# Kernel tuning notes

Hardware: AMD Instinct MI355X
Metric: run time of the kernel (lower is better)

## Reference

```python
import jax, jax.numpy as jnp
import numpy as np

B, W, D, R = 8, 1024, 1024, 64
GAMMA_MIN, GAMMA_MAX, ALPHA_CAP, EPS = 0.15, 1.0, 1.0, 1e-8


def _linear_init(key, fan_in, shape):
    bound = 1.0 / np.sqrt(fan_in)
    return jax.random.uniform(key, shape, jnp.float32, -bound, bound)


def setup_inputs() -> dict:
    key = jax.random.key(0)
    ks = jax.random.split(key, 12)
    h = jax.random.normal(ks[0], (B, W, D), jnp.float32)
    # k_base init as in __init__: exp(-0.15*max(j-i,0)) * tril, row-normalized
    pos = jnp.arange(W, dtype=jnp.float32)
    dist_ji = jnp.clip(pos[None, :] - pos[:, None], 0.0)
    causal = jnp.tril(jnp.ones((W, W), jnp.float32))
    k_init = jnp.exp(-0.15 * dist_ji) * causal
    k_base = k_init / jnp.clip(k_init.sum(axis=1, keepdims=True), 1e-8)
    # decay_logit init: gammas in [0.95, 0.995] -> inverse sigmoid of normalized gamma
    gammas = jnp.linspace(0.95, 0.995, R)
    graw = jnp.clip((gammas - GAMMA_MIN) / (GAMMA_MAX - GAMMA_MIN), 1e-6, 1 - 1e-6)
    decay_logit = jnp.log(graw / (1.0 - graw))
    return {
        "h": h,
        "k_base": k_base,
        "decay_logit": decay_logit,
        "gate_logit": jnp.asarray(8.0, jnp.float32),
        "alpha_logit": jnp.asarray(0.0, jnp.float32),
        "u": 0.05 * jax.random.normal(ks[1], (D, R), jnp.float32),
        "v": 0.05 * jax.random.normal(ks[2], (D, R), jnp.float32),
        "proj_w": _linear_init(ks[3], D, (D, D)),
        "proj_b": _linear_init(ks[4], D, (D,)),
        "norm1_scale": jnp.ones((D,), jnp.float32),
        "norm2_scale": jnp.ones((D,), jnp.float32),
        "up_w": _linear_init(ks[5], D, (2 * D, D)),
        "up_b": _linear_init(ks[6], D, (2 * D,)),
        "down_w": _linear_init(ks[7], 2 * D, (D, 2 * D)),
        "down_b": _linear_init(ks[8], 2 * D, (D,)),
    }


def _rmsnorm(x, scale):
    return x * jax.lax.rsqrt(jnp.mean(x * x, axis=-1, keepdims=True) + 1e-8) * scale


def _l2norm(x):
    # mirrors F.normalize(x, dim=-1, eps=1e-8)
    n = jnp.sqrt(jnp.sum(x * x, axis=-1, keepdims=True))
    return x / jnp.maximum(n, EPS)


def reference(h, k_base, decay_logit, gate_logit, alpha_logit, u, v,
              proj_w, proj_b, norm1_scale, norm2_scale,
              up_w, up_b, down_w, down_b):
    _, w, _ = h.shape
    pos = jnp.arange(w, dtype=h.dtype)
    causal = jnp.tril(jnp.ones((w, w), h.dtype))          # [W, W]
    dist = jnp.clip(pos[:, None] - pos[None, :], 0.0)     # i - j, clamped >= 0

    residual = h
    h_norm = _rmsnorm(h, norm1_scale)

    # dense k_base path (k_base_rank == 0)
    gate = jax.nn.sigmoid(gate_logit)
    kb = k_base[:w, :w] * causal
    out = gate * jnp.einsum('ij,bjd->bid', kb, h_norm)

    # low-rank q/k with per-rank gamma decay (decay_impl='mask')
    qk = h_norm @ jnp.concatenate((u, v), axis=1)          # [B, W, 2R]
    q_raw, k_raw = jnp.split(qk, [u.shape[1]], axis=-1)
    q = _l2norm(q_raw)
    k = _l2norm(k_raw)

    gamma = GAMMA_MIN + (GAMMA_MAX - GAMMA_MIN) * jax.nn.sigmoid(decay_logit)  # [R]
    log_gamma = jnp.log(jnp.clip(gamma, 1e-8))
    decay_mask = jnp.exp(dist[:, :, None] * log_gamma[None, None, :]) * causal[:, :, None]  # [W, W, R]

    alpha = ALPHA_CAP * jax.nn.sigmoid(alpha_logit)
    # scores[b,i,j] = sum_r q[b,i,r] * decay[i,j,r] * k[b,j,r]
    scores = jnp.einsum('bir,ijr,bjr->bij', q, decay_mask, k)
    out = out + alpha * jnp.einsum('bij,bjd->bid', scores, h_norm)

    h1 = residual + (out @ proj_w.T + proj_b)
    # MLP (GELU exact, mult=2), second residual
    m = _rmsnorm(h1, norm2_scale)
    m = jax.nn.gelu(m @ up_w.T + up_b, approximate=False) @ down_w.T + down_b
    return h1 + m
```

## Files before the change

### kernel.cpp

```cpp
#include <hip/hip_runtime.h>
#include <hip/hip_bf16.h>
#include <math.h>

#define B_ 8
#define W_ 1024
#define D_ 1024
#define R_ 64

typedef __hip_bfloat16 bf16;
typedef __attribute__((ext_vector_type(8))) short bf16x8;
typedef __attribute__((ext_vector_type(4))) float f32x4;

__device__ __forceinline__ float tof(bf16 x) { return __bfloat162float(x); }
__device__ __forceinline__ short f2bs(float f) {
    bf16 b = __float2bfloat16(f);
    return *(short*)&b;
}

__device__ __forceinline__ void async16(const void* g, void* l) {
    __builtin_amdgcn_global_load_lds(
        (const __attribute__((address_space(1))) unsigned int*)g,
        (__attribute__((address_space(3))) unsigned int*)l,
        16, 0, 0);
}

__global__ __launch_bounds__(256)
void rmsnorm_kernel(const float* __restrict__ src, const float* __restrict__ scale,
                    bf16* __restrict__ dst) {
    int row = blockIdx.x;
    const float* x = src + (size_t)row * D_;
    bf16* y = dst + (size_t)row * D_;
    float xv[4];
    float ss = 0.f;
#pragma unroll
    for (int it = 0; it < 4; ++it) {
        int d = threadIdx.x + it * 256;
        xv[it] = x[d];
        ss += xv[it] * xv[it];
    }
#pragma unroll
    for (int off = 32; off; off >>= 1) ss += __shfl_down(ss, off, 64);
    __shared__ float red[4];
    __shared__ float invs;
    int lane = threadIdx.x & 63, wid = threadIdx.x >> 6;
    if (lane == 0) red[wid] = ss;
    __syncthreads();
    if (threadIdx.x == 0) {
        float t = red[0] + red[1] + red[2] + red[3];
        invs = rsqrtf(t / (float)D_ + 1e-8f);
    }
    __syncthreads();
    float inv = invs;
#pragma unroll
    for (int it = 0; it < 4; ++it) {
        int d = threadIdx.x + it * 256;
        y[d] = __float2bfloat16(xv[it] * inv * scale[d]);
    }
}

__global__ __launch_bounds__(256)
void transpose_kernel(const bf16* __restrict__ src, bf16* __restrict__ dst) {
    int b = blockIdx.z;
    int j0 = blockIdx.x * 64, d0 = blockIdx.y * 64;
    __shared__ short Ts[64][72];
    const bf16* S = src + (size_t)b * W_ * D_;
    bf16* Dd = dst + (size_t)b * W_ * D_;
    int tid = threadIdx.x;
    int r = tid >> 3, c = (tid & 7) * 8;
#pragma unroll
    for (int p = 0; p < 2; ++p) {
        int j = r + p * 32;
        bf16x8 vv = *(const bf16x8*)&S[(size_t)(j0 + j) * D_ + d0 + c];
#pragma unroll
        for (int e = 0; e < 8; ++e) Ts[j][c + e] = vv[e];
    }
    __syncthreads();
#pragma unroll
    for (int p = 0; p < 2; ++p) {
        int d = r + p * 32;
        bf16x8 vv;
#pragma unroll
        for (int e = 0; e < 8; ++e) vv[e] = Ts[c + e][d];
        *(bf16x8*)&Dd[(size_t)(d0 + d) * W_ + j0 + c] = vv;
    }
}

__global__ __launch_bounds__(256)
void uvT_kernel(const float* __restrict__ u, const float* __restrict__ v,
                bf16* __restrict__ uvT) {
    int g = blockIdx.z;
    int d0 = blockIdx.x * 64;
    const float* src = g ? v : u;
    __shared__ float Ts[64][65];
    int tid = threadIdx.x;
#pragma unroll
    for (int e = 0; e < 16; ++e) {
        int idx = tid + e * 256;
        int drow = idx >> 6, rcol = idx & 63;
        Ts[drow][rcol] = src[(size_t)(d0 + drow) * 64 + rcol];
    }
    __syncthreads();
#pragma unroll
    for (int e = 0; e < 16; ++e) {
        int idx = tid + e * 256;
        int orow = idx >> 6, ocol = idx & 63;
        uvT[(size_t)(g * 64 + orow) * D_ + d0 + ocol] = __float2bfloat16(Ts[ocol][orow]);
    }
}

__global__ __launch_bounds__(256)
void convert3_kernel(const float* __restrict__ proj, const float* __restrict__ up,
                     const float* __restrict__ down,
                     bf16* __restrict__ projb, bf16* __restrict__ upb,
                     bf16* __restrict__ downb) {
    size_t idx = ((size_t)blockIdx.x * 256 + threadIdx.x) * 8;
    const size_t DD = (size_t)D_ * D_;
    const float* src; bf16* dst; size_t off;
    if (idx < DD)          { src = proj; dst = projb; off = idx; }
    else if (idx < 3 * DD) { src = up;   dst = upb;   off = idx - DD; }
    else                   { src = down; dst = downb; off = idx - 3 * DD; }
    float4 f0 = *(const float4*)(src + off);
    float4 f1 = *(const float4*)(src + off + 4);
    bf16x8 p;
    p[0] = f2bs(f0.x); p[1] = f2bs(f0.y); p[2] = f2bs(f0.z); p[3] = f2bs(f0.w);
    p[4] = f2bs(f1.x); p[5] = f2bs(f1.y); p[6] = f2bs(f1.z); p[7] = f2bs(f1.w);
    *(bf16x8*)(dst + off) = p;
}

__global__ __launch_bounds__(128)
void qk_epilogue_kernel(const float* __restrict__ qkraw,
                        const float* __restrict__ decay_logit,
                        float* __restrict__ qg, float* __restrict__ kg) {
    int row = blockIdx.x;
    int i = row & (W_ - 1);
    int t = threadIdx.x;
    int r = t & 63;
    bool isK = t >= 64;
    const size_t PS = (size_t)B_ * W_ * 128;
    size_t off = (size_t)row * 128 + t;
    float val = qkraw[off] + qkraw[PS + off] + qkraw[2 * PS + off] + qkraw[3 * PS + off];
    float sq = val * val;
#pragma unroll
    for (int o = 32; o; o >>= 1) sq += __shfl_xor(sq, o, 64);
    val = val / fmaxf(sqrtf(sq), 1e-8f);

    float dl = decay_logit[r];
    float gamma = 0.15f + 0.85f * (1.f / (1.f + expf(-dl)));
    float lg = logf(gamma);
    float e = isK ? expf(-(float)i * lg) : expf((float)i * lg);
    float o = val * e;
    if (isK) kg[(size_t)row * R_ + r] = o;
    else     qg[(size_t)row * R_ + r] = o;
}

__global__ __launch_bounds__(256)
void buildM_kernel(const float* __restrict__ qg, const float* __restrict__ kg,
                   const float* __restrict__ k_base,
                   const float* __restrict__ gate_logit,
                   const float* __restrict__ alpha_logit,
                   bf16* __restrict__ M) {
    int b = blockIdx.z;
    int ti = blockIdx.y, tj = blockIdx.x;
    int i0 = ti * 32, j0 = tj * 32;
    int tx = threadIdx.x, ty = threadIdx.y;
    bf16* Mb = M + (size_t)b * W_ * W_;
    const bf16 zero = __float2bfloat16(0.f);

    if (tj > ti) {
#pragma unroll
        for (int a = 0; a < 2; ++a)
#pragma unroll
            for (int c = 0; c < 2; ++c)
                Mb[(size_t)(i0 + ty * 2 + a) * W_ + (j0 + tx * 2 + c)] = zero;
        return;
    }

    __shared__ float Qs[32][65];
    __shared__ float Ks[32][65];
    int tid = ty * 16 + tx;
    for (int e = tid; e < 32 * 64; e += 256) {
        int rr = e & 63, row = e >> 6;
        Qs[row][rr] = qg[((size_t)b * W_ + i0 + row) * R_ + rr];
        Ks[row][rr] = kg[((size_t)b * W_ + j0 + row) * R_ + rr];
    }
    __syncthreads();

    float acc[2][2] = {{0.f, 0.f}, {0.f, 0.f}};
#pragma unroll 8
    for (int r = 0; r < 64; ++r) {
        float qa = Qs[ty * 2 + 0][r], qb = Qs[ty * 2 + 1][r];
        float ka = Ks[tx * 2 + 0][r], kb = Ks[tx * 2 + 1][r];
        acc[0][0] += qa * ka; acc[0][1] += qa * kb;
        acc[1][0] += qb * ka; acc[1][1] += qb * kb;
    }

    float gate  = 1.f / (1.f + expf(-(*gate_logit)));
    float alpha = 1.f / (1.f + expf(-(*alpha_logit)));
#pragma unroll
    for (int a = 0; a < 2; ++a) {
#pragma unroll
        for (int c = 0; c < 2; ++c) {
            int i = i0 + ty * 2 + a, j = j0 + tx * 2 + c;
            float vkb = k_base[(size_t)i * W_ + j];
            float out = (j <= i) ? (gate * vkb + alpha * acc[a][c]) : 0.f;
            Mb[(size_t)i * W_ + j] = __float2bfloat16(out);
        }
    }
}

#define BAR() do { __builtin_amdgcn_sched_barrier(0); \
                   __builtin_amdgcn_s_barrier(); \
                   __builtin_amdgcn_sched_barrier(0); } while (0)

__device__ __forceinline__ void mfma8(const bf16x8 (&fa)[2], const bf16x8 (&fb)[4],
                                      f32x4 (&acc)[2][4]) {
#pragma unroll
    for (int mi = 0; mi < 2; ++mi)
#pragma unroll
        for (int ni = 0; ni < 4; ++ni)
            acc[mi][ni] = __builtin_amdgcn_mfma_f32_16x16x32_bf16(
                fa[mi], fb[ni], acc[mi][ni], 0, 0, 0);
}

__device__ __forceinline__ void readf(const short* At0, const short* Bt0, int slot,
                                      const int (&ao)[2], const int (&bo)[4],
                                      bf16x8 (&fa)[2], bf16x8 (&fb)[4]) {
    const short* Ard = At0 + slot * 4096;
    const short* Brd = Bt0 + slot * 4096;
#pragma unroll
    for (int mi = 0; mi < 2; ++mi) fa[mi] = *(const bf16x8*)&Ard[ao[mi]];
#pragma unroll
    for (int ni = 0; ni < 4; ++ni) fb[ni] = *(const bf16x8*)&Brd[bo[ni]];
}

template<int EPI, int SK>
__global__ __launch_bounds__(512, 4)
void mgemm_kernel(const bf16* __restrict__ A, const bf16* __restrict__ Bm,
                  const float* __restrict__ Res, const float* __restrict__ bias,
                  void* __restrict__ Cout,
                  int M, int N, int K,
                  long sA, long sB, long sC, int causal) {
    __shared__ __align__(16) short At[5][128 * 32];
    __shared__ __align__(16) short Bt[5][128 * 32];
    int z = blockIdx.z;
    const bf16* Ab = (SK > 1) ? A : A + (size_t)z * sA;
    const bf16* Bb = (SK > 1) ? Bm : Bm + (size_t)z * sB;
    int kchunk = K / SK;
    int kbeg = (SK > 1) ? z * kchunk : 0;
    int m0 = blockIdx.x * 128, n0 = blockIdx.y * 128;
    int tid = threadIdx.x;
    int lane = tid & 63, wave = tid >> 6;
    int wy = wave >> 1, wx = wave & 1;
    int quad = lane >> 4, l15 = lane & 15;

    f32x4 acc[2][4];
#pragma unroll
    for (int i = 0; i < 2; ++i)
#pragma unroll
        for (int j = 0; j < 4; ++j)
            acc[i][j] = (f32x4){0.f, 0.f, 0.f, 0.f};

    int kend = kbeg + kchunk;
    if (SK == 1 && causal) kend = (m0 + 128 < K) ? m0 + 128 : K;
    int nIter = (kend - kbeg) >> 5;

    int srcChunk = ((lane & 3) ^ ((lane >> 3) & 3)) * 8;
    size_t rowA = (size_t)(m0 + wave * 16 + (lane >> 2)) * K;
    size_t rowB = (size_t)(n0 + wave * 16 + (lane >> 2)) * K;
    const bf16* aP = Ab + rowA + srcChunk + kbeg;
    const bf16* bP = Bb + rowB + srcChunk + kbeg;
    short* aDst = &At[0][0] + wave * 512;
    short* bDst = &Bt[0][0] + wave * 512;

    int rswz = (quad ^ ((l15 >> 1) & 3)) * 8;
    int ao[2], bo[4];
#pragma unroll
    for (int mi = 0; mi < 2; ++mi) ao[mi] = (wy * 32 + mi * 16 + l15) * 32 + rswz;
#pragma unroll
    for (int ni = 0; ni < 4; ++ni) bo[ni] = (wx * 64 + ni * 16 + l15) * 32 + rswz;

#pragma unroll
    for (int p = 0; p < 4; ++p) {
        async16(aP, aDst + p * 4096);
        async16(bP, bDst + p * 4096);
        aP += 32; bP += 32;
    }
    asm volatile("s_waitcnt vmcnt(6)" ::: "memory");
    BAR();

    bf16x8 fa0[2], fb0[4], fa1[2], fb1[4];
    readf(&At[0][0], &Bt[0][0], 0, ao, bo, fa0, fb0);

    int sStage = 4;
    int sPf = 1;
    int nMain = nIter - 4;

    for (int t = 0; t < nMain; t += 2) {
        asm volatile("s_waitcnt vmcnt(4)" ::: "memory");
        BAR();
        async16(aP, aDst + sStage * 4096);
        async16(bP, bDst + sStage * 4096);
        aP += 32; bP += 32;
        sStage = (sStage == 4) ? 0 : sStage + 1;
        mfma8(fa0, fb0, acc);
        readf(&At[0][0], &Bt[0][0], sPf, ao, bo, fa1, fb1);
        sPf = (sPf == 4) ? 0 : sPf + 1;
        asm volatile("s_waitcnt vmcnt(4)" ::: "memory");
        BAR();
        async16(aP, aDst + sStage * 4096);
        async16(bP, bDst + sStage * 4096);
        aP += 32; bP += 32;
        sStage = (sStage == 4) ? 0 : sStage + 1;
        mfma8(fa1, fb1, acc);
        readf(&At[0][0], &Bt[0][0], sPf, ao, bo, fa0, fb0);
        sPf = (sPf == 4) ? 0 : sPf + 1;
    }

    asm volatile("s_waitcnt vmcnt(4)" ::: "memory");
    BAR();
    mfma8(fa0, fb0, acc);
    readf(&At[0][0], &Bt[0][0], sPf, ao, bo, fa1, fb1);
    sPf = (sPf == 4) ? 0 : sPf + 1;

    asm volatile("s_waitcnt vmcnt(2)" ::: "memory");
    BAR();
    mfma8(fa1, fb1, acc);
    readf(&At[0][0], &Bt[0][0], sPf, ao, bo, fa0, fb0);
    sPf = (sPf == 4) ? 0 : sPf + 1;

    asm volatile("s_waitcnt vmcnt(0)" ::: "memory");
    BAR();
    mfma8(fa0, fb0, acc);
    readf(&At[0][0], &Bt[0][0], sPf, ao, bo, fa1, fb1);

    mfma8(fa1, fb1, acc);

#pragma unroll
    for (int ni = 0; ni < 4; ++ni) {
        int col = n0 + wx * 64 + ni * 16 + l15;
        float bv = (EPI == 1 || EPI == 2) ? bias[col] : 0.f;
#pragma unroll
        for (int mi = 0; mi < 2; ++mi) {
            int row0 = m0 + wy * 32 + mi * 16 + quad * 4;
#pragma unroll
            for (int r = 0; r < 4; ++r) {
                size_t idx = (size_t)(row0 + r) * N + col;
                float val = acc[mi][ni][r];
                if constexpr (EPI == 0) {
                    ((bf16*)Cout)[(size_t)z * sC + idx] = __float2bfloat16(val);
                } else if constexpr (EPI == 1) {
                    ((float*)Cout)[idx] = val + bv + Res[idx];
                } else if constexpr (EPI == 2) {
                    val += bv;
                    val = 0.5f * val * (1.f + erff(val * 0.70710678118654752f));
                    ((bf16*)Cout)[idx] = __float2bfloat16(val);
                } else {
                    ((float*)Cout)[(size_t)z * sC + idx] = val;
                }
            }
        }
    }
}

__device__ __forceinline__ void mfma16(const bf16x8 (&fa)[4], const bf16x8 (&fb)[4],
                                       f32x4 (&acc)[4][4]) {
#pragma unroll
    for (int mi = 0; mi < 4; ++mi)
#pragma unroll
        for (int ni = 0; ni < 4; ++ni)
            acc[mi][ni] = __builtin_amdgcn_mfma_f32_16x16x32_bf16(
                fa[mi], fb[ni], acc[mi][ni], 0, 0, 0);
}

template<int EPI>
__global__ __launch_bounds__(512, 4)
void mgemm2_kernel(const bf16* __restrict__ A, const bf16* __restrict__ Bm,
                   const float* __restrict__ Res, const float* __restrict__ bias,
                   void* __restrict__ Cout,
                   int M, int N, int K, long sA, long sB, long sC, int causal) {
    __shared__ __align__(16) short At[3][256 * 32];
    __shared__ __align__(16) short Bt[3][128 * 32];
    int z = blockIdx.z;
    const bf16* Ab = A + (size_t)z * sA;
    const bf16* Bb = Bm + (size_t)z * sB;

    int bx = blockIdx.x, gx = gridDim.x;
    if ((gx & 7) == 0) { int cpx = gx >> 3; bx = (bx & 7) * cpx + (bx >> 3); }
    int m0 = bx * 256, n0 = blockIdx.y * 128;

    int tid = threadIdx.x;
    int lane = tid & 63, wave = tid >> 6;
    int wm = wave >> 1, wn = wave & 1;
    int quad = lane >> 4, l15 = lane & 15;

    f32x4 acc[4][4];
#pragma unroll
    for (int i = 0; i < 4; ++i)
#pragma unroll
        for (int j = 0; j < 4; ++j)
            acc[i][j] = (f32x4){0.f, 0.f, 0.f, 0.f};

    int kend = causal ? ((m0 + 256 < K) ? m0 + 256 : K) : K;
    int nIter = kend >> 5;

    int srcChunk = ((lane & 3) ^ ((lane >> 3) & 3)) * 8;
    size_t rowA0 = (size_t)(m0 + wave * 32 + (lane >> 2)) * K;
    size_t rowB  = (size_t)(n0 + wave * 16 + (lane >> 2)) * K;
    const bf16* aP0 = Ab + rowA0 + srcChunk;
    const bf16* aP1 = aP0 + (size_t)16 * K;
    const bf16* bP  = Bb + rowB + srcChunk;
    short* aDst = &At[0][0] + wave * 1024;
    short* bDst = &Bt[0][0] + wave * 512;

    int rswz = (quad ^ ((l15 >> 1) & 3)) * 8;
    int ao[4], bo[4];
#pragma unroll
    for (int mi = 0; mi < 4; ++mi) ao[mi] = (wm * 64 + mi * 16 + l15) * 32 + rswz;
#pragma unroll
    for (int ni = 0; ni < 4; ++ni) bo[ni] = (wn * 64 + ni * 16 + l15) * 32 + rswz;

    async16(aP0, aDst);
    async16(aP1, aDst + 512);
    async16(bP,  bDst);
    aP0 += 32; aP1 += 32; bP += 32;
    if (nIter > 1) {
        async16(aP0, aDst + 8192);
        async16(aP1, aDst + 8192 + 512);
        async16(bP,  bDst + 4096);
        aP0 += 32; aP1 += 32; bP += 32;
        asm volatile("s_waitcnt vmcnt(3)" ::: "memory");
    } else {
        asm volatile("s_waitcnt vmcnt(0)" ::: "memory");
    }
    BAR();

    int sCur = 0;
    int sStage = 2;

    for (int t = 0; t < nIter; ++t) {
        bool i2 = (t + 2 < nIter);
        if (i2) {
            async16(aP0, aDst + sStage * 8192);
            async16(aP1, aDst + sStage * 8192 + 512);
            async16(bP,  bDst + sStage * 4096);
            aP0 += 32; aP1 += 32; bP += 32;
            sStage = (sStage == 2) ? 0 : sStage + 1;
        }
        bf16x8 fa[4], fb[4];
        const short* Ard = &At[0][0] + sCur * 8192;
        const short* Brd = &Bt[0][0] + sCur * 4096;
#pragma unroll
        for (int mi = 0; mi < 4; ++mi) fa[mi] = *(const bf16x8*)&Ard[ao[mi]];
#pragma unroll
        for (int ni = 0; ni < 4; ++ni) fb[ni] = *(const bf16x8*)&Brd[bo[ni]];
        mfma16(fa, fb, acc);
        if (t + 1 < nIter) {
            if (i2) asm volatile("s_waitcnt vmcnt(3)" ::: "memory");
            else    asm volatile("s_waitcnt vmcnt(0)" ::: "memory");
            BAR();
            sCur = (sCur == 2) ? 0 : sCur + 1;
        }
    }

#pragma unroll
    for (int ni = 0; ni < 4; ++ni) {
        int col = n0 + wn * 64 + ni * 16 + l15;
        float bv = (EPI == 1 || EPI == 2) ? bias[col] : 0.f;
#pragma unroll
        for (int mi = 0; mi < 4; ++mi) {
            int row0 = m0 + wm * 64 + mi * 16 + quad * 4;
#pragma unroll
            for (int r = 0; r < 4; ++r) {
                size_t idx = (size_t)(row0 + r) * N + col;
                float val = acc[mi][ni][r];
                if constexpr (EPI == 0) {
                    ((bf16*)Cout)[(size_t)z * sC + idx] = __float2bfloat16(val);
                } else if constexpr (EPI == 1) {
                    ((float*)Cout)[idx] = val + bv + Res[idx];
                } else {
                    val += bv;
                    val = 0.5f * val * (1.f + erff(val * 0.70710678118654752f));
                    ((bf16*)Cout)[idx] = __float2bfloat16(val);
                }
            }
        }
    }
}

extern "C" void kernel_launch(void* const* d_in, const int* in_sizes, int n_in,
                              void* d_out, int out_size, void* d_ws, size_t ws_size,
                              hipStream_t stream) {
    const float* h           = (const float*)d_in[0];
    const float* k_base      = (const float*)d_in[1];
    const float* decay_logit = (const float*)d_in[2];
    const float* gate_logit  = (const float*)d_in[3];
    const float* alpha_logit = (const float*)d_in[4];
    const float* u           = (const float*)d_in[5];
    const float* v           = (const float*)d_in[6];
    const float* proj_w      = (const float*)d_in[7];
    const float* proj_b      = (const float*)d_in[8];
    const float* norm1_scale = (const float*)d_in[9];
    const float* norm2_scale = (const float*)d_in[10];
    const float* up_w        = (const float*)d_in[11];
    const float* up_b        = (const float*)d_in[12];
    const float* down_w      = (const float*)d_in[13];
    const float* down_b      = (const float*)d_in[14];

    const size_t MB = 1048576;
    char* ws = (char*)d_ws;
    bf16*  hnorm   = (bf16*)(ws);
    bf16*  uvT     = (bf16*)(ws + 16 * MB);
    float* qg      = (float*)(ws + 16 * MB);
    float* kg      = (float*)(ws + 18 * MB);
    bf16*  hnormT  = (bf16*)(ws + 20 * MB);
    float* qkraw   = (float*)(ws + 36 * MB);
    bf16*  Mbuf    = (bf16*)(ws + 36 * MB);
    bf16*  proj_wb = (bf16*)(ws + 52 * MB);
    bf16*  up_wb   = (bf16*)(ws + 54 * MB);
    bf16*  down_wb = (bf16*)(ws + 58 * MB);
    bf16*  attn    = hnorm;
    bf16*  mnorm   = hnorm;
    bf16*  tbuf    = hnormT;
    float* h1      = (float*)d_out;

    convert3_kernel<<<5 * D_ * D_ / 2048, 256, 0, stream>>>(
        proj_w, up_w, down_w, proj_wb, up_wb, down_wb);
    uvT_kernel<<<dim3(D_ / 64, 1, 2), 256, 0, stream>>>(u, v, uvT);

    rmsnorm_kernel<<<B_ * W_, 256, 0, stream>>>(h, norm1_scale, hnorm);

    transpose_kernel<<<dim3(W_ / 64, D_ / 64, B_), 256, 0, stream>>>(hnorm, hnormT);

    mgemm_kernel<5, 4><<<dim3(B_ * W_ / 128, 1, 4), 512, 0, stream>>>(
        hnorm, uvT, nullptr, nullptr, qkraw, B_ * W_, 128, D_,
        0, 0, (long)B_ * W_ * 128, 0);

    qk_epilogue_kernel<<<B_ * W_, 128, 0, stream>>>(qkraw, decay_logit, qg, kg);

    buildM_kernel<<<dim3(W_ / 32, W_ / 32, B_), dim3(16, 16), 0, stream>>>(
        qg, kg, k_base, gate_logit, alpha_logit, Mbuf);

    mgemm2_kernel<0><<<dim3(W_ / 256, D_ / 128, B_), 512, 0, stream>>>(
        Mbuf, hnormT, nullptr, nullptr, attn, W_, D_, W_,
        (long)W_ * W_, (long)W_ * D_, (long)W_ * D_, 1);

    mgemm2_kernel<1><<<dim3(B_ * W_ / 256, D_ / 128, 1), 512, 0, stream>>>(
        attn, proj_wb, h, proj_b, h1, B_ * W_, D_, D_, 0, 0, 0, 0);

    rmsnorm_kernel<<<B_ * W_, 256, 0, stream>>>(h1, norm2_scale, mnorm);

    mgemm2_kernel<2><<<dim3(B_ * W_ / 256, 2 * D_ / 128, 1), 512, 0, stream>>>(
        mnorm, up_wb, nullptr, up_b, tbuf, B_ * W_, 2 * D_, D_, 0, 0, 0, 0);

    mgemm2_kernel<1><<<dim3(B_ * W_ / 256, D_ / 128, 1), 512, 0, stream>>>(
        tbuf, down_wb, h1, down_b, (float*)d_out, B_ * W_, D_, 2 * D_, 0, 0, 0, 0);
}
```

Baseline: 373.4 us.

## Replace 256x128 GEMM with 128x128 4-wave kernel using 4-stage ping-pong fragment prefetch

```diff
diff --git a/kernel.cpp b/kernel.cpp
--- a/kernel.cpp
+++ b/kernel.cpp
@@ -229,6 +229,27 @@
     const short* Brd = Bt0 + slot * 4096;
 #pragma unroll
     for (int mi = 0; mi < 2; ++mi) fa[mi] = *(const bf16x8*)&Ard[ao[mi]];
+#pragma unroll
+    for (int ni = 0; ni < 4; ++ni) fb[ni] = *(const bf16x8*)&Brd[bo[ni]];
+}
+
+__device__ __forceinline__ void mfma16(const bf16x8 (&fa)[4], const bf16x8 (&fb)[4],
+                                       f32x4 (&acc)[4][4]) {
+#pragma unroll
+    for (int mi = 0; mi < 4; ++mi)
+#pragma unroll
+        for (int ni = 0; ni < 4; ++ni)
+            acc[mi][ni] = __builtin_amdgcn_mfma_f32_16x16x32_bf16(
+                fa[mi], fb[ni], acc[mi][ni], 0, 0, 0);
+}
+
+__device__ __forceinline__ void readf4(const short* At0, const short* Bt0, int slot,
+                                       const int (&ao)[4], const int (&bo)[4],
+                                       bf16x8 (&fa)[4], bf16x8 (&fb)[4]) {
+    const short* Ard = At0 + slot * 4096;
+    const short* Brd = Bt0 + slot * 4096;
+#pragma unroll
+    for (int mi = 0; mi < 4; ++mi) fa[mi] = *(const bf16x8*)&Ard[ao[mi]];
 #pragma unroll
     for (int ni = 0; ni < 4; ++ni) fb[ni] = *(const bf16x8*)&Brd[bo[ni]];
 }
@@ -362,31 +383,21 @@
     }
 }
 
-__device__ __forceinline__ void mfma16(const bf16x8 (&fa)[4], const bf16x8 (&fb)[4],
-                                       f32x4 (&acc)[4][4]) {
-#pragma unroll
-    for (int mi = 0; mi < 4; ++mi)
-#pragma unroll
-        for (int ni = 0; ni < 4; ++ni)
-            acc[mi][ni] = __builtin_amdgcn_mfma_f32_16x16x32_bf16(
-                fa[mi], fb[ni], acc[mi][ni], 0, 0, 0);
-}
-
 template<int EPI>
-__global__ __launch_bounds__(512, 4)
-void mgemm2_kernel(const bf16* __restrict__ A, const bf16* __restrict__ Bm,
+__global__ __launch_bounds__(256, 2)
+void mgemm3_kernel(const bf16* __restrict__ A, const bf16* __restrict__ Bm,
                    const float* __restrict__ Res, const float* __restrict__ bias,
                    void* __restrict__ Cout,
                    int M, int N, int K, long sA, long sB, long sC, int causal) {
-    __shared__ __align__(16) short At[3][256 * 32];
-    __shared__ __align__(16) short Bt[3][128 * 32];
+    __shared__ __align__(16) short At[4][128 * 32];
+    __shared__ __align__(16) short Bt[4][128 * 32];
     int z = blockIdx.z;
     const bf16* Ab = A + (size_t)z * sA;
     const bf16* Bb = Bm + (size_t)z * sB;
 
     int bx = blockIdx.x, gx = gridDim.x;
     if ((gx & 7) == 0) { int cpx = gx >> 3; bx = (bx & 7) * cpx + (bx >> 3); }
-    int m0 = bx * 256, n0 = blockIdx.y * 128;
+    int m0 = bx * 128, n0 = blockIdx.y * 128;
 
     int tid = threadIdx.x;
     int lane = tid & 63, wave = tid >> 6;
@@ -400,17 +411,16 @@
         for (int j = 0; j < 4; ++j)
             acc[i][j] = (f32x4){0.f, 0.f, 0.f, 0.f};
 
-    int kend = causal ? ((m0 + 256 < K) ? m0 + 256 : K) : K;
+    int kend = causal ? ((m0 + 128 < K) ? m0 + 128 : K) : K;
     int nIter = kend >> 5;
 
     int srcChunk = ((lane & 3) ^ ((lane >> 3) & 3)) * 8;
-    size_t rowA0 = (size_t)(m0 + wave * 32 + (lane >> 2)) * K;
-    size_t rowB  = (size_t)(n0 + wave * 16 + (lane >> 2)) * K;
-    const bf16* aP0 = Ab + rowA0 + srcChunk;
+    const bf16* aP0 = Ab + (size_t)(m0 + wave * 32 + (lane >> 2)) * K + srcChunk;
     const bf16* aP1 = aP0 + (size_t)16 * K;
-    const bf16* bP  = Bb + rowB + srcChunk;
+    const bf16* bP0 = Bb + (size_t)(n0 + wave * 32 + (lane >> 2)) * K + srcChunk;
+    const bf16* bP1 = bP0 + (size_t)16 * K;
     short* aDst = &At[0][0] + wave * 1024;
-    short* bDst = &Bt[0][0] + wave * 512;
+    short* bDst = &Bt[0][0] + wave * 1024;
 
     int rswz = (quad ^ ((l15 >> 1) & 3)) * 8;
     int ao[4], bo[4];
@@ -419,48 +429,47 @@
 #pragma unroll
     for (int ni = 0; ni < 4; ++ni) bo[ni] = (wn * 64 + ni * 16 + l15) * 32 + rswz;
 
-    async16(aP0, aDst);
-    async16(aP1, aDst + 512);
-    async16(bP,  bDst);
-    aP0 += 32; aP1 += 32; bP += 32;
-    if (nIter > 1) {
-        async16(aP0, aDst + 8192);
-        async16(aP1, aDst + 8192 + 512);
-        async16(bP,  bDst + 4096);
-        aP0 += 32; aP1 += 32; bP += 32;
-        asm volatile("s_waitcnt vmcnt(3)" ::: "memory");
-    } else {
-        asm volatile("s_waitcnt vmcnt(0)" ::: "memory");
-    }
+#define STG3(slot) do { \
+        short* _a = aDst + (slot) * 4096; \
+        short* _b = bDst + (slot) * 4096; \
+        async16(aP0, _a); async16(aP1, _a + 512); \
+        async16(bP0, _b); async16(bP1, _b + 512); \
+        aP0 += 32; aP1 += 32; bP0 += 32; bP1 += 32; \
+    } while (0)
+
+    STG3(0); STG3(1); STG3(2);
+    asm volatile("s_waitcnt vmcnt(8)" ::: "memory");
     BAR();
 
-    int sCur = 0;
-    int sStage = 2;
-
-    for (int t = 0; t < nIter; ++t) {
-        bool i2 = (t + 2 < nIter);
-        if (i2) {
-            async16(aP0, aDst + sStage * 8192);
-            async16(aP1, aDst + sStage * 8192 + 512);
-            async16(bP,  bDst + sStage * 4096);
-            aP0 += 32; aP1 += 32; bP += 32;
-            sStage = (sStage == 2) ? 0 : sStage + 1;
-        }
-        bf16x8 fa[4], fb[4];
-        const short* Ard = &At[0][0] + sCur * 8192;
-        const short* Brd = &Bt[0][0] + sCur * 4096;
-#pragma unroll
-        for (int mi = 0; mi < 4; ++mi) fa[mi] = *(const bf16x8*)&Ard[ao[mi]];
-#pragma unroll
-        for (int ni = 0; ni < 4; ++ni) fb[ni] = *(const bf16x8*)&Brd[bo[ni]];
-        mfma16(fa, fb, acc);
-        if (t + 1 < nIter) {
-            if (i2) asm volatile("s_waitcnt vmcnt(3)" ::: "memory");
-            else    asm volatile("s_waitcnt vmcnt(0)" ::: "memory");
-            BAR();
-            sCur = (sCur == 2) ? 0 : sCur + 1;
-        }
-    }
+    bf16x8 fa0[4], fb0[4], fa1[4], fb1[4];
+    readf4(&At[0][0], &Bt[0][0], 0, ao, bo, fa0, fb0);
+
+    int sStage = 3;
+    int sPf = 1;
+    int nMain = nIter - 2;
+
+    for (int t = 0; t < nMain; t += 2) {
+        asm volatile("s_waitcnt vmcnt(4)" ::: "memory");
+        BAR();
+        if (t + 3 < nIter) { STG3(sStage & 3); ++sStage; }
+        mfma16(fa0, fb0, acc);
+        readf4(&At[0][0], &Bt[0][0], sPf & 3, ao, bo, fa1, fb1);
+        ++sPf;
+        if (t + 3 < nIter) asm volatile("s_waitcnt vmcnt(4)" ::: "memory");
+        else               asm volatile("s_waitcnt vmcnt(0)" ::: "memory");
+        BAR();
+        if (t + 4 < nIter) { STG3(sStage & 3); ++sStage; }
+        mfma16(fa1, fb1, acc);
+        readf4(&At[0][0], &Bt[0][0], sPf & 3, ao, bo, fa0, fb0);
+        ++sPf;
+    }
+
+    asm volatile("s_waitcnt vmcnt(0)" ::: "memory");
+    BAR();
+    mfma16(fa0, fb0, acc);
+    readf4(&At[0][0], &Bt[0][0], sPf & 3, ao, bo, fa1, fb1);
+    mfma16(fa1, fb1, acc);
+#undef STG3
 
 #pragma unroll
     for (int ni = 0; ni < 4; ++ni) {
@@ -540,18 +549,18 @@
     buildM_kernel<<<dim3(W_ / 32, W_ / 32, B_), dim3(16, 16), 0, stream>>>(
         qg, kg, k_base, gate_logit, alpha_logit, Mbuf);
 
-    mgemm2_kernel<0><<<dim3(W_ / 256, D_ / 128, B_), 512, 0, stream>>>(
+    mgemm3_kernel<0><<<dim3(W_ / 128, D_ / 128, B_), 256, 0, stream>>>(
         Mbuf, hnormT, nullptr, nullptr, attn, W_, D_, W_,
         (long)W_ * W_, (long)W_ * D_, (long)W_ * D_, 1);
 
-    mgemm2_kernel<1><<<dim3(B_ * W_ / 256, D_ / 128, 1), 512, 0, stream>>>(
+    mgemm3_kernel<1><<<dim3(B_ * W_ / 128, D_ / 128, 1), 256, 0, stream>>>(
         attn, proj_wb, h, proj_b, h1, B_ * W_, D_, D_, 0, 0, 0, 0);
 
     rmsnorm_kernel<<<B_ * W_, 256, 0, stream>>>(h1, norm2_scale, mnorm);
 
-    mgemm2_kernel<2><<<dim3(B_ * W_ / 256, 2 * D_ / 128, 1), 512, 0, stream>>>(
+    mgemm3_kernel<2><<<dim3(B_ * W_ / 128, 2 * D_ / 128, 1), 256, 0, stream>>>(
         mnorm, up_wb, nullptr, up_b, tbuf, B_ * W_, 2 * D_, D_, 0, 0, 0, 0);
 
-    mgemm2_kernel<1><<<dim3(B_ * W_ / 256, D_ / 128, 1), 512, 0, stream>>>(
+    mgemm3_kernel<1><<<dim3(B_ * W_ / 128, D_ / 128, 1), 256, 0, stream>>>(
         tbuf, down_wb, h1, down_b, (float*)d_out, B_ * W_, D_, 2 * D_, 0, 0, 0, 0);
 }
```

Result: faster. 356.3 us (-4.6%).
